# Optimization experiments

Hardware: AMD Instinct MI355X
Metric: run time of the kernel (lower is better)

The kernel has to match this reference:

```python
import jax, jax.numpy as jnp
import numpy as np

N_NODES = 20000

def gcn(h, W, b, src, dst):
    # DGL GraphConv, norm='both': D_out^-1/2 on src, aggregate, D_in^-1/2 on dst, then W, b
    E = src.shape[0]
    ones = jnp.ones((E,), dtype=h.dtype)
    out_deg = jnp.clip(jax.ops.segment_sum(ones, src, N_NODES), 1.0)
    in_deg = jnp.clip(jax.ops.segment_sum(ones, dst, N_NODES), 1.0)
    dn_src = jax.lax.rsqrt(out_deg)  # [N]
    dn_dst = jax.lax.rsqrt(in_deg)
    hs = h * dn_src[None, :, None]           # [B,N,H]
    msg = hs[:, src, :]                      # [B,E,H] gather
    agg = jax.vmap(lambda m: jax.ops.segment_sum(m, dst, N_NODES))(msg)  # [B,N,H]
    agg = agg * dn_dst[None, :, None]
    return agg @ W + b

def setup_inputs() -> dict:
    key = jax.random.key(0)
    ks = jax.random.split(key, 16)
    B, N, H, I, E = 4, N_NODES, 128, 64, 320000
    inp = {
        'x': jax.random.normal(ks[0], (B, I), jnp.float32),
        'h_prev': jax.random.normal(ks[1], (B, N, H), jnp.float32),
        'c_prev': jax.random.normal(ks[2], (B, N, H), jnp.float32),
        'src': jax.random.randint(ks[3], (E,), 0, N, jnp.int32),
        'dst': jax.random.randint(ks[4], (E,), 0, N, jnp.int32),
    }
    s_in = 1.0 / np.sqrt(I)
    s_h = 1.0 / np.sqrt(H)
    inp['Wi'] = jax.random.uniform(ks[5], (I, H), jnp.float32, -s_in, s_in)
    inp['bi'] = jax.random.uniform(ks[6], (H,), jnp.float32, -s_in, s_in)
    inp['Wf'] = jax.random.uniform(ks[7], (I, H), jnp.float32, -s_in, s_in)
    inp['bf'] = jax.random.uniform(ks[8], (H,), jnp.float32, -s_in, s_in)
    inp['Wo'] = jax.random.uniform(ks[9], (I, H), jnp.float32, -s_in, s_in)
    inp['bo'] = jax.random.uniform(ks[10], (H,), jnp.float32, -s_in, s_in)
    inp['Wc'] = jax.random.uniform(ks[11], (I, H), jnp.float32, -s_in, s_in)
    inp['bc'] = jax.random.uniform(ks[12], (H,), jnp.float32, -s_in, s_in)
    inp['Wg'] = jax.random.uniform(ks[13], (H, H), jnp.float32, -s_h, s_h)
    inp['bg'] = jax.random.uniform(ks[14], (H,), jnp.float32, -s_h, s_h)
    return inp

def reference(x, h_prev, c_prev, src, dst, Wi, bi, Wf, bf, Wo, bo, Wc, bc, Wg, bg):
    # gcn_h(g, h_prev) is identical in all four gates -> compute once
    gh = gcn(h_prev, Wg, bg, src, dst)  # [B,N,H]
    i_t = jax.nn.sigmoid((x @ Wi + bi)[:, None, :] + gh)
    f_t = jax.nn.sigmoid((x @ Wf + bf)[:, None, :] + gh)
    o_t = jax.nn.sigmoid((x @ Wo + bo)[:, None, :] + gh)
    c_tilde = jnp.tanh((x @ Wc + bc)[:, None, :] + gh)
    c_t = f_t * c_prev + i_t * c_tilde
    h_t = o_t * jnp.tanh(c_t)
    return h_t, c_t
```

## Files before the change

kernel.cpp:

```cpp
#include <hip/hip_runtime.h>
#include <hip/hip_bf16.h>

#define N_NODES 20000
#define B 4
#define H 128
#define I_DIM 64
#define E_MAX 320000
#define CAP 64

typedef __attribute__((ext_vector_type(8))) short short8;
typedef __attribute__((ext_vector_type(4))) float float4v;

__device__ int   g_cnt_dst[N_NODES];
__device__ int   g_deg_src[N_NODES];
__device__ int   g_csr[N_NODES * CAP];
__device__ float g_xg[4 * B * H];
__device__ __align__(16) uint2 g_hs[N_NODES * H];
__device__ __align__(16) unsigned short g_wgB[H * H];

__global__ __launch_bounds__(256)
void degree_kernel(const int* __restrict__ src, int E, int eb,
                   const float* __restrict__ x,
                   const float* __restrict__ Wi, const float* __restrict__ bi,
                   const float* __restrict__ Wf, const float* __restrict__ bf_,
                   const float* __restrict__ Wo, const float* __restrict__ bo,
                   const float* __restrict__ Wc, const float* __restrict__ bc,
                   const float* __restrict__ Wg) {
    int blk = blockIdx.x;
    int t = threadIdx.x;
    if (blk < eb) {
        int e = blk * 256 + t;
        if (e < E) atomicAdd(&g_deg_src[src[e]], 1);
    } else if (blk < eb + 8) {
        int bid = blk - eb;
        int g = bid >> 1;
        int b = ((bid & 1) << 1) | (t >> 7);
        int h = t & 127;
        const float* W;
        const float* bb;
        switch (g) {
            case 0: W = Wi; bb = bi; break;
            case 1: W = Wf; bb = bf_; break;
            case 2: W = Wo; bb = bo; break;
            default: W = Wc; bb = bc; break;
        }
        float acc = bb[h];
#pragma unroll
        for (int i = 0; i < I_DIM; i++)
            acc += x[b * I_DIM + i] * W[i * H + h];
        g_xg[(g * B + b) * H + h] = acc;
    } else {
        int i = (blk - eb - 8) * 256 + t;
        int tn = i >> 11;
        int rem = i & 2047;
        int kb = rem >> 9;
        int rem2 = rem & 511;
        int lane = rem2 >> 3;
        int j = rem2 & 7;
        int k  = kb * 32 + (lane >> 4) * 8 + j;
        int nn = tn * 16 + (lane & 15);
        __hip_bfloat16 hv = __float2bfloat16(Wg[k * H + nn]);
        g_wgB[i] = *reinterpret_cast<unsigned short*>(&hv);
    }
}

__global__ __launch_bounds__(256)
void mid_kernel(const float* __restrict__ h_prev,
                const int* __restrict__ src, const int* __restrict__ dst, int E) {
    const int PACK_BLKS = (N_NODES * H) / 256;
    int blk = blockIdx.x;
    int t = threadIdx.x;

    if (blk < PACK_BLKS) {
        int i = blk * 256 + t;
        int n = i >> 7;
        float sc = rsqrtf(fmaxf((float)g_deg_src[n], 1.0f));
        const long stride = (long)N_NODES * H;
        float v0 = h_prev[i] * sc;
        float v1 = h_prev[i + stride] * sc;
        float v2 = h_prev[i + 2 * stride] * sc;
        float v3 = h_prev[i + 3 * stride] * sc;
        __hip_bfloat162 p01 = __float22bfloat162_rn(make_float2(v0, v1));
        __hip_bfloat162 p23 = __float22bfloat162_rn(make_float2(v2, v3));
        uint2 wv;
        wv.x = *reinterpret_cast<unsigned int*>(&p01);
        wv.y = *reinterpret_cast<unsigned int*>(&p23);
        g_hs[i] = wv;
    } else {
        int e = (blk - PACK_BLKS) * 256 + t;
        if (e < E) {
            int d = dst[e];
            int slot = atomicAdd(&g_cnt_dst[d], 1);
            if (slot < CAP) g_csr[(d << 6) + slot] = src[e];
        }
    }
}

__device__ __forceinline__ float fast_sigmoid(float z) {
    return 1.f / (1.f + __expf(-z));
}
__device__ __forceinline__ float fast_tanh(float z) {
    return 1.f - 2.f / (__expf(2.f * z) + 1.f);
}
__device__ __forceinline__ unsigned pack2bf(float lo, float hi) {
    __hip_bfloat162 p = __float22bfloat162_rn(make_float2(lo, hi));
    return *reinterpret_cast<unsigned*>(&p);
}

__global__ __launch_bounds__(256)
void fused_kernel(const float* __restrict__ bg,
                  const float* __restrict__ c_prev,
                  float* __restrict__ out_h, float* __restrict__ out_c) {
    int t = threadIdx.x;
    int w = t >> 6;
    int lane = t & 63;
    int n = (blockIdx.x << 2) + w;
    const long stride = (long)N_NODES * H;

    int cnt = g_cnt_dst[n];
    float dd = rsqrtf(fmaxf((float)cnt, 1.0f));
    if (cnt > CAP) cnt = CAP;

    __shared__ int sbase[4][64];
    __shared__ unsigned short Atile[16][136];

    sbase[w][lane] = g_csr[(n << 6) + (lane < cnt ? lane : 0)] << 6;

    float cpr[2][4];
    {
        long ne = (long)((blockIdx.x << 2) + (lane >> 4));
#pragma unroll
        for (int i = 0; i < 2; i++) {
            int h = (2 * w + i) * 16 + (lane & 15);
#pragma unroll
            for (int j = 0; j < 4; j++)
                cpr[i][j] = __builtin_nontemporal_load(
                    &c_prev[(long)j * stride + ne * H + h]);
        }
    }

    float a0 = 0.f, a1 = 0.f, a2 = 0.f, a3 = 0.f;
    float a4 = 0.f, a5 = 0.f, a6 = 0.f, a7 = 0.f;
    const uint4* hs4 = reinterpret_cast<const uint4*>(g_hs);
    const int* sb = sbase[w];

#define ACCV(v) { \
        __hip_bfloat162 p; float2 f; \
        p = *reinterpret_cast<__hip_bfloat162*>(&(v).x); f = __bfloat1622float2(p); a0 += f.x; a1 += f.y; \
        p = *reinterpret_cast<__hip_bfloat162*>(&(v).y); f = __bfloat1622float2(p); a2 += f.x; a3 += f.y; \
        p = *reinterpret_cast<__hip_bfloat162*>(&(v).z); f = __bfloat1622float2(p); a4 += f.x; a5 += f.y; \
        p = *reinterpret_cast<__hip_bfloat162*>(&(v).w); f = __bfloat1622float2(p); a6 += f.x; a7 += f.y; }

    int j = 0;
    for (; j + 8 <= cnt; j += 8) {
        int b0 = sb[j];
        int b1 = sb[j + 1];
        int b2 = sb[j + 2];
        int b3 = sb[j + 3];
        int b4 = sb[j + 4];
        int b5 = sb[j + 5];
        int b6 = sb[j + 6];
        int b7 = sb[j + 7];
        uint4 v0 = hs4[b0 + lane];
        uint4 v1 = hs4[b1 + lane];
        uint4 v2 = hs4[b2 + lane];
        uint4 v3 = hs4[b3 + lane];
        uint4 v4 = hs4[b4 + lane];
        uint4 v5 = hs4[b5 + lane];
        uint4 v6 = hs4[b6 + lane];
        uint4 v7 = hs4[b7 + lane];
        ACCV(v0); ACCV(v1); ACCV(v2); ACCV(v3);
        ACCV(v4); ACCV(v5); ACCV(v6); ACCV(v7);
    }
    for (; j < cnt; j++) {
        uint4 v = hs4[sb[j] + lane];
        ACCV(v);
    }
#undef ACCV

    *reinterpret_cast<unsigned*>(&Atile[w * 4 + 0][2 * lane]) = pack2bf(a0 * dd, a4 * dd);
    *reinterpret_cast<unsigned*>(&Atile[w * 4 + 1][2 * lane]) = pack2bf(a1 * dd, a5 * dd);
    *reinterpret_cast<unsigned*>(&Atile[w * 4 + 2][2 * lane]) = pack2bf(a2 * dd, a6 * dd);
    *reinterpret_cast<unsigned*>(&Atile[w * 4 + 3][2 * lane]) = pack2bf(a3 * dd, a7 * dd);

    __syncthreads();

    if (t < 4)                 g_cnt_dst[(blockIdx.x << 2) + t] = 0;
    else if (t >= 64 && t < 68) g_deg_src[(blockIdx.x << 2) + (t - 64)] = 0;

    int arow = lane & 15;
    int agrp = lane >> 4;
    float4v c0 = {0.f, 0.f, 0.f, 0.f};
    float4v c1 = {0.f, 0.f, 0.f, 0.f};
#pragma unroll
    for (int kb = 0; kb < 4; kb++) {
        short8 af = *reinterpret_cast<const short8*>(&Atile[arow][kb * 32 + agrp * 8]);
        short8 bf0 = *reinterpret_cast<const short8*>(
            &g_wgB[(((2 * w) * 4 + kb) * 64 + lane) * 8]);
        short8 bf1 = *reinterpret_cast<const short8*>(
            &g_wgB[(((2 * w + 1) * 4 + kb) * 64 + lane) * 8]);
        c0 = __builtin_amdgcn_mfma_f32_16x16x32_bf16(af, bf0, c0, 0, 0, 0);
        c1 = __builtin_amdgcn_mfma_f32_16x16x32_bf16(af, bf1, c1, 0, 0, 0);
    }

    long ne = (long)((blockIdx.x << 2) + (lane >> 4));
#pragma unroll
    for (int i = 0; i < 2; i++) {
        float4v c = i ? c1 : c0;
        int h = (2 * w + i) * 16 + (lane & 15);
        float bgh = bg[h];
#pragma unroll
        for (int jj = 0; jj < 4; jj++) {
            float gh = c[jj] + bgh;
            float xi = g_xg[(0 * B + jj) * H + h];
            float xf = g_xg[(1 * B + jj) * H + h];
            float xo = g_xg[(2 * B + jj) * H + h];
            float xc = g_xg[(3 * B + jj) * H + h];

            float it = fast_sigmoid(xi + gh);
            float ft = fast_sigmoid(xf + gh);
            float ot = fast_sigmoid(xo + gh);
            float ct = fast_tanh(xc + gh);

            float cc = ft * cpr[i][jj] + it * ct;
            float ho = ot * fast_tanh(cc);

            long idx = (long)jj * stride + ne * H + h;
            __builtin_nontemporal_store(ho, &out_h[idx]);
            __builtin_nontemporal_store(cc, &out_c[idx]);
        }
    }
}

extern "C" void kernel_launch(void* const* d_in, const int* in_sizes, int n_in,
                              void* d_out, int out_size, void* d_ws, size_t ws_size,
                              hipStream_t stream) {
    const float* x      = (const float*)d_in[0];
    const float* h_prev = (const float*)d_in[1];
    const float* c_prev = (const float*)d_in[2];
    const int* src = (const int*)d_in[3];
    const int* dst = (const int*)d_in[4];
    const float* Wi = (const float*)d_in[5];
    const float* bi = (const float*)d_in[6];
    const float* Wf = (const float*)d_in[7];
    const float* bf_ = (const float*)d_in[8];
    const float* Wo = (const float*)d_in[9];
    const float* bo = (const float*)d_in[10];
    const float* Wc = (const float*)d_in[11];
    const float* bc = (const float*)d_in[12];
    const float* Wg = (const float*)d_in[13];
    const float* bg = (const float*)d_in[14];

    int E = in_sizes[3];
    if (E > E_MAX) E = E_MAX;
    int eb = (E + 255) / 256;
    const int PACK_BLKS = (N_NODES * H) / 256;

    degree_kernel<<<eb + 8 + 64, 256, 0, stream>>>(src, E, eb,
        x, Wi, bi, Wf, bf_, Wo, bo, Wc, bc, Wg);
    mid_kernel<<<PACK_BLKS + eb, 256, 0, stream>>>(h_prev, src, dst, E);

    float* out_h = (float*)d_out;
    float* out_c = out_h + (long)B * N_NODES * H;
    fused_kernel<<<N_NODES / 4, 256, 0, stream>>>(bg, c_prev, out_h, out_c);
}
```

Baseline: 263.2 us.

## Give each wavefront four nodes with full-width MFMA and no block barrier

Each wavefront now gathers neighbour features for four destination nodes and runs the whole 16x128 MFMA tile on its own, so the block-wide __syncthreads is gone and the grid shrinks by four. The gather loop is unrolled to 16 loads, c_prev loads are placed between gather phases to overlap, and the gate inputs are stored interleaved so one float4 load replaces four scalar loads. The cost is higher register pressure (eight accumulator tiles plus 32 cached c_prev values), which may lower occupancy, and fewer blocks overall.

```diff
diff --git a/kernel.cpp b/kernel.cpp
--- a/kernel.cpp
+++ b/kernel.cpp
@@ -14,7 +14,7 @@
 __device__ int   g_cnt_dst[N_NODES];
 __device__ int   g_deg_src[N_NODES];
 __device__ int   g_csr[N_NODES * CAP];
-__device__ float g_xg[4 * B * H];
+__device__ __align__(16) float g_xg[4 * B * H];
 __device__ __align__(16) uint2 g_hs[N_NODES * H];
 __device__ __align__(16) unsigned short g_wgB[H * H];
 
@@ -48,7 +48,7 @@
 #pragma unroll
         for (int i = 0; i < I_DIM; i++)
             acc += x[b * I_DIM + i] * W[i * H + h];
-        g_xg[(g * B + b) * H + h] = acc;
+        g_xg[(b * H + h) * 4 + g] = acc;
     } else {
         int i = (blk - eb - 8) * 256 + t;
         int tn = i >> 11;
@@ -114,33 +114,32 @@
     int t = threadIdx.x;
     int w = t >> 6;
     int lane = t & 63;
-    int n = (blockIdx.x << 2) + w;
+    int q = (blockIdx.x * 4 + w) * 4;
     const long stride = (long)N_NODES * H;
 
-    int cnt = g_cnt_dst[n];
-    float dd = rsqrtf(fmaxf((float)cnt, 1.0f));
-    if (cnt > CAP) cnt = CAP;
-
-    __shared__ int sbase[4][64];
-    __shared__ unsigned short Atile[16][136];
-
-    sbase[w][lane] = g_csr[(n << 6) + (lane < cnt ? lane : 0)] << 6;
-
-    float cpr[2][4];
+    __shared__ int            sbase[4][4 * 64];
+    __shared__ unsigned short Atile[4][16][136];
+
+    int cnt0 = g_cnt_dst[q + 0];
+    int cnt1 = g_cnt_dst[q + 1];
+    int cnt2 = g_cnt_dst[q + 2];
+    int cnt3 = g_cnt_dst[q + 3];
+    float dd0 = rsqrtf(fmaxf((float)cnt0, 1.0f)); if (cnt0 > CAP) cnt0 = CAP;
+    float dd1 = rsqrtf(fmaxf((float)cnt1, 1.0f)); if (cnt1 > CAP) cnt1 = CAP;
+    float dd2 = rsqrtf(fmaxf((float)cnt2, 1.0f)); if (cnt2 > CAP) cnt2 = CAP;
+    float dd3 = rsqrtf(fmaxf((float)cnt3, 1.0f)); if (cnt3 > CAP) cnt3 = CAP;
+
     {
-        long ne = (long)((blockIdx.x << 2) + (lane >> 4));
-#pragma unroll
-        for (int i = 0; i < 2; i++) {
-            int h = (2 * w + i) * 16 + (lane & 15);
-#pragma unroll
-            for (int j = 0; j < 4; j++)
-                cpr[i][j] = __builtin_nontemporal_load(
-                    &c_prev[(long)j * stride + ne * H + h]);
-        }
-    }
-
-    float a0 = 0.f, a1 = 0.f, a2 = 0.f, a3 = 0.f;
-    float a4 = 0.f, a5 = 0.f, a6 = 0.f, a7 = 0.f;
+        int s0 = g_csr[((q + 0) << 6) + (lane < cnt0 ? lane : 0)];
+        int s1 = g_csr[((q + 1) << 6) + (lane < cnt1 ? lane : 0)];
+        int s2 = g_csr[((q + 2) << 6) + (lane < cnt2 ? lane : 0)];
+        int s3 = g_csr[((q + 3) << 6) + (lane < cnt3 ? lane : 0)];
+        sbase[w][0 * 64 + lane] = s0 << 6;
+        sbase[w][1 * 64 + lane] = s1 << 6;
+        sbase[w][2 * 64 + lane] = s2 << 6;
+        sbase[w][3 * 64 + lane] = s3 << 6;
+    }
+
     const uint4* hs4 = reinterpret_cast<const uint4*>(g_hs);
     const int* sb = sbase[w];
 
@@ -151,84 +150,112 @@
         p = *reinterpret_cast<__hip_bfloat162*>(&(v).z); f = __bfloat1622float2(p); a4 += f.x; a5 += f.y; \
         p = *reinterpret_cast<__hip_bfloat162*>(&(v).w); f = __bfloat1622float2(p); a6 += f.x; a7 += f.y; }
 
-    int j = 0;
-    for (; j + 8 <= cnt; j += 8) {
-        int b0 = sb[j];
-        int b1 = sb[j + 1];
-        int b2 = sb[j + 2];
-        int b3 = sb[j + 3];
-        int b4 = sb[j + 4];
-        int b5 = sb[j + 5];
-        int b6 = sb[j + 6];
-        int b7 = sb[j + 7];
-        uint4 v0 = hs4[b0 + lane];
-        uint4 v1 = hs4[b1 + lane];
-        uint4 v2 = hs4[b2 + lane];
-        uint4 v3 = hs4[b3 + lane];
-        uint4 v4 = hs4[b4 + lane];
-        uint4 v5 = hs4[b5 + lane];
-        uint4 v6 = hs4[b6 + lane];
-        uint4 v7 = hs4[b7 + lane];
-        ACCV(v0); ACCV(v1); ACCV(v2); ACCV(v3);
-        ACCV(v4); ACCV(v5); ACCV(v6); ACCV(v7);
-    }
-    for (; j < cnt; j++) {
-        uint4 v = hs4[sb[j] + lane];
-        ACCV(v);
-    }
+#define GATHER_NODE(i, cnt, dd) { \
+        float a0 = 0.f, a1 = 0.f, a2 = 0.f, a3 = 0.f; \
+        float a4 = 0.f, a5 = 0.f, a6 = 0.f, a7 = 0.f; \
+        int j = 0; \
+        for (; j + 16 <= (cnt); j += 16) { \
+            int b0 = sb[(i) * 64 + j];      int b1 = sb[(i) * 64 + j + 1]; \
+            int b2 = sb[(i) * 64 + j + 2];  int b3 = sb[(i) * 64 + j + 3]; \
+            int b4 = sb[(i) * 64 + j + 4];  int b5 = sb[(i) * 64 + j + 5]; \
+            int b6 = sb[(i) * 64 + j + 6];  int b7 = sb[(i) * 64 + j + 7]; \
+            int b8 = sb[(i) * 64 + j + 8];  int b9 = sb[(i) * 64 + j + 9]; \
+            int b10 = sb[(i) * 64 + j + 10]; int b11 = sb[(i) * 64 + j + 11]; \
+            int b12 = sb[(i) * 64 + j + 12]; int b13 = sb[(i) * 64 + j + 13]; \
+            int b14 = sb[(i) * 64 + j + 14]; int b15 = sb[(i) * 64 + j + 15]; \
+            uint4 v0 = hs4[b0 + lane];   uint4 v1 = hs4[b1 + lane]; \
+            uint4 v2 = hs4[b2 + lane];   uint4 v3 = hs4[b3 + lane]; \
+            uint4 v4 = hs4[b4 + lane];   uint4 v5 = hs4[b5 + lane]; \
+            uint4 v6 = hs4[b6 + lane];   uint4 v7 = hs4[b7 + lane]; \
+            uint4 v8 = hs4[b8 + lane];   uint4 v9 = hs4[b9 + lane]; \
+            uint4 v10 = hs4[b10 + lane]; uint4 v11 = hs4[b11 + lane]; \
+            uint4 v12 = hs4[b12 + lane]; uint4 v13 = hs4[b13 + lane]; \
+            uint4 v14 = hs4[b14 + lane]; uint4 v15 = hs4[b15 + lane]; \
+            ACCV(v0);  ACCV(v1);  ACCV(v2);  ACCV(v3); \
+            ACCV(v4);  ACCV(v5);  ACCV(v6);  ACCV(v7); \
+            ACCV(v8);  ACCV(v9);  ACCV(v10); ACCV(v11); \
+            ACCV(v12); ACCV(v13); ACCV(v14); ACCV(v15); \
+        } \
+        for (; j + 4 <= (cnt); j += 4) { \
+            int b0 = sb[(i) * 64 + j];     int b1 = sb[(i) * 64 + j + 1]; \
+            int b2 = sb[(i) * 64 + j + 2]; int b3 = sb[(i) * 64 + j + 3]; \
+            uint4 v0 = hs4[b0 + lane]; uint4 v1 = hs4[b1 + lane]; \
+            uint4 v2 = hs4[b2 + lane]; uint4 v3 = hs4[b3 + lane]; \
+            ACCV(v0); ACCV(v1); ACCV(v2); ACCV(v3); \
+        } \
+        for (; j < (cnt); j++) { \
+            uint4 v = hs4[sb[(i) * 64 + j] + lane]; \
+            ACCV(v); \
+        } \
+        *reinterpret_cast<unsigned*>(&Atile[w][(i) * 4 + 0][2 * lane]) = pack2bf(a0 * (dd), a4 * (dd)); \
+        *reinterpret_cast<unsigned*>(&Atile[w][(i) * 4 + 1][2 * lane]) = pack2bf(a1 * (dd), a5 * (dd)); \
+        *reinterpret_cast<unsigned*>(&Atile[w][(i) * 4 + 2][2 * lane]) = pack2bf(a2 * (dd), a6 * (dd)); \
+        *reinterpret_cast<unsigned*>(&Atile[w][(i) * 4 + 3][2 * lane]) = pack2bf(a3 * (dd), a7 * (dd)); \
+    }
+
+    GATHER_NODE(0, cnt0, dd0);
+    GATHER_NODE(1, cnt1, dd1);
+
+    int hl = lane & 15;
+    long ne = (long)(q + (lane >> 4));
+    float cpr[8][4];
+#pragma unroll
+    for (int tn = 0; tn < 8; tn++) {
+        int h = tn * 16 + hl;
+#pragma unroll
+        for (int jj = 0; jj < 4; jj++)
+            cpr[tn][jj] = __builtin_nontemporal_load(
+                &c_prev[(long)jj * stride + ne * H + h]);
+    }
+
+    GATHER_NODE(2, cnt2, dd2);
+    GATHER_NODE(3, cnt3, dd3);
+#undef GATHER_NODE
 #undef ACCV
-
-    *reinterpret_cast<unsigned*>(&Atile[w * 4 + 0][2 * lane]) = pack2bf(a0 * dd, a4 * dd);
-    *reinterpret_cast<unsigned*>(&Atile[w * 4 + 1][2 * lane]) = pack2bf(a1 * dd, a5 * dd);
-    *reinterpret_cast<unsigned*>(&Atile[w * 4 + 2][2 * lane]) = pack2bf(a2 * dd, a6 * dd);
-    *reinterpret_cast<unsigned*>(&Atile[w * 4 + 3][2 * lane]) = pack2bf(a3 * dd, a7 * dd);
-
-    __syncthreads();
-
-    if (t < 4)                 g_cnt_dst[(blockIdx.x << 2) + t] = 0;
-    else if (t >= 64 && t < 68) g_deg_src[(blockIdx.x << 2) + (t - 64)] = 0;
 
     int arow = lane & 15;
     int agrp = lane >> 4;
-    float4v c0 = {0.f, 0.f, 0.f, 0.f};
-    float4v c1 = {0.f, 0.f, 0.f, 0.f};
+    float4v c[8];
+#pragma unroll
+    for (int tn = 0; tn < 8; tn++) c[tn] = (float4v){0.f, 0.f, 0.f, 0.f};
 #pragma unroll
     for (int kb = 0; kb < 4; kb++) {
-        short8 af = *reinterpret_cast<const short8*>(&Atile[arow][kb * 32 + agrp * 8]);
-        short8 bf0 = *reinterpret_cast<const short8*>(
-            &g_wgB[(((2 * w) * 4 + kb) * 64 + lane) * 8]);
-        short8 bf1 = *reinterpret_cast<const short8*>(
-            &g_wgB[(((2 * w + 1) * 4 + kb) * 64 + lane) * 8]);
-        c0 = __builtin_amdgcn_mfma_f32_16x16x32_bf16(af, bf0, c0, 0, 0, 0);
-        c1 = __builtin_amdgcn_mfma_f32_16x16x32_bf16(af, bf1, c1, 0, 0, 0);
-    }
-
-    long ne = (long)((blockIdx.x << 2) + (lane >> 4));
-#pragma unroll
-    for (int i = 0; i < 2; i++) {
-        float4v c = i ? c1 : c0;
-        int h = (2 * w + i) * 16 + (lane & 15);
+        short8 af = *reinterpret_cast<const short8*>(&Atile[w][arow][kb * 32 + agrp * 8]);
+#pragma unroll
+        for (int tn = 0; tn < 8; tn++) {
+            short8 bf = *reinterpret_cast<const short8*>(
+                &g_wgB[((tn * 4 + kb) * 64 + lane) * 8]);
+            c[tn] = __builtin_amdgcn_mfma_f32_16x16x32_bf16(af, bf, c[tn], 0, 0, 0);
+        }
+    }
+
+    const float4* xg4 = reinterpret_cast<const float4*>(g_xg);
+#pragma unroll
+    for (int tn = 0; tn < 8; tn++) {
+        int h = tn * 16 + hl;
         float bgh = bg[h];
 #pragma unroll
         for (int jj = 0; jj < 4; jj++) {
-            float gh = c[jj] + bgh;
-            float xi = g_xg[(0 * B + jj) * H + h];
-            float xf = g_xg[(1 * B + jj) * H + h];
-            float xo = g_xg[(2 * B + jj) * H + h];
-            float xc = g_xg[(3 * B + jj) * H + h];
-
-            float it = fast_sigmoid(xi + gh);
-            float ft = fast_sigmoid(xf + gh);
-            float ot = fast_sigmoid(xo + gh);
-            float ct = fast_tanh(xc + gh);
-
-            float cc = ft * cpr[i][jj] + it * ct;
+            float gh = c[tn][jj] + bgh;
+            float4 xv = xg4[jj * H + h];
+
+            float it = fast_sigmoid(xv.x + gh);
+            float ft = fast_sigmoid(xv.y + gh);
+            float ot = fast_sigmoid(xv.z + gh);
+            float ct = fast_tanh(xv.w + gh);
+
+            float cc = ft * cpr[tn][jj] + it * ct;
             float ho = ot * fast_tanh(cc);
 
             long idx = (long)jj * stride + ne * H + h;
             __builtin_nontemporal_store(ho, &out_h[idx]);
             __builtin_nontemporal_store(cc, &out_c[idx]);
         }
+    }
+
+    if (lane < 4) {
+        g_cnt_dst[q + lane] = 0;
+        g_deg_src[q + lane] = 0;
     }
 }
 
@@ -262,5 +289,5 @@
 
     float* out_h = (float*)d_out;
     float* out_c = out_h + (long)B * N_NODES * H;
-    fused_kernel<<<N_NODES / 4, 256, 0, stream>>>(bg, c_prev, out_h, out_c);
-}
+    fused_kernel<<<N_NODES / 16, 256, 0, stream>>>(bg, c_prev, out_h, out_c);
+}
```

After: 279.6 us. +6.2%, slower.

## Make each wave compute its own node's GEMM to drop block barrier

Applied to the files above, without the earlier changes.

Each wave now keeps a private A tile filled with its own node's four batch rows replicated across sixteen rows. It runs all eight N-tiles of the Wg matmul itself, so the block-wide __syncthreads is gone and the counter resets happen per wave. The gate inputs g_xg are re-laid out so the four gate values for a (batch, h) pair come in one float4 load, and a 4-wide tail loop is added to the gather. The cost is four times the MFMA work and B-fragment loads per wave, most of it spent on redundant rows, plus four times the shared memory.

```diff
diff --git a/kernel.cpp b/kernel.cpp
--- a/kernel.cpp
+++ b/kernel.cpp
@@ -14,7 +14,7 @@
 __device__ int   g_cnt_dst[N_NODES];
 __device__ int   g_deg_src[N_NODES];
 __device__ int   g_csr[N_NODES * CAP];
-__device__ float g_xg[4 * B * H];
+__device__ __align__(16) float g_xg[4 * B * H];
 __device__ __align__(16) uint2 g_hs[N_NODES * H];
 __device__ __align__(16) unsigned short g_wgB[H * H];
 
@@ -48,7 +48,7 @@
 #pragma unroll
         for (int i = 0; i < I_DIM; i++)
             acc += x[b * I_DIM + i] * W[i * H + h];
-        g_xg[(g * B + b) * H + h] = acc;
+        g_xg[(b * H + h) * 4 + g] = acc;
     } else {
         int i = (blk - eb - 8) * 256 + t;
         int tn = i >> 11;
@@ -117,27 +117,22 @@
     int n = (blockIdx.x << 2) + w;
     const long stride = (long)N_NODES * H;
 
+    __shared__ int            sbase[4][64];
+    __shared__ unsigned short Atile[4][16][136];
+
     int cnt = g_cnt_dst[n];
     float dd = rsqrtf(fmaxf((float)cnt, 1.0f));
     if (cnt > CAP) cnt = CAP;
 
-    __shared__ int sbase[4][64];
-    __shared__ unsigned short Atile[16][136];
-
     sbase[w][lane] = g_csr[(n << 6) + (lane < cnt ? lane : 0)] << 6;
 
     float cpr[2][4];
-    {
-        long ne = (long)((blockIdx.x << 2) + (lane >> 4));
-#pragma unroll
-        for (int i = 0; i < 2; i++) {
-            int h = (2 * w + i) * 16 + (lane & 15);
-#pragma unroll
-            for (int j = 0; j < 4; j++)
-                cpr[i][j] = __builtin_nontemporal_load(
-                    &c_prev[(long)j * stride + ne * H + h]);
-        }
-    }
+#pragma unroll
+    for (int half = 0; half < 2; half++)
+#pragma unroll
+        for (int jj = 0; jj < 4; jj++)
+            cpr[half][jj] = __builtin_nontemporal_load(
+                &c_prev[(long)jj * stride + (long)n * H + 64 * half + lane]);
 
     float a0 = 0.f, a1 = 0.f, a2 = 0.f, a3 = 0.f;
     float a4 = 0.f, a5 = 0.f, a6 = 0.f, a7 = 0.f;
@@ -153,24 +148,23 @@
 
     int j = 0;
     for (; j + 8 <= cnt; j += 8) {
-        int b0 = sb[j];
-        int b1 = sb[j + 1];
-        int b2 = sb[j + 2];
-        int b3 = sb[j + 3];
-        int b4 = sb[j + 4];
-        int b5 = sb[j + 5];
-        int b6 = sb[j + 6];
-        int b7 = sb[j + 7];
-        uint4 v0 = hs4[b0 + lane];
-        uint4 v1 = hs4[b1 + lane];
-        uint4 v2 = hs4[b2 + lane];
-        uint4 v3 = hs4[b3 + lane];
-        uint4 v4 = hs4[b4 + lane];
-        uint4 v5 = hs4[b5 + lane];
-        uint4 v6 = hs4[b6 + lane];
-        uint4 v7 = hs4[b7 + lane];
+        int b0 = sb[j];     int b1 = sb[j + 1];
+        int b2 = sb[j + 2]; int b3 = sb[j + 3];
+        int b4 = sb[j + 4]; int b5 = sb[j + 5];
+        int b6 = sb[j + 6]; int b7 = sb[j + 7];
+        uint4 v0 = hs4[b0 + lane]; uint4 v1 = hs4[b1 + lane];
+        uint4 v2 = hs4[b2 + lane]; uint4 v3 = hs4[b3 + lane];
+        uint4 v4 = hs4[b4 + lane]; uint4 v5 = hs4[b5 + lane];
+        uint4 v6 = hs4[b6 + lane]; uint4 v7 = hs4[b7 + lane];
         ACCV(v0); ACCV(v1); ACCV(v2); ACCV(v3);
         ACCV(v4); ACCV(v5); ACCV(v6); ACCV(v7);
+    }
+    for (; j + 4 <= cnt; j += 4) {
+        int b0 = sb[j];     int b1 = sb[j + 1];
+        int b2 = sb[j + 2]; int b3 = sb[j + 3];
+        uint4 v0 = hs4[b0 + lane]; uint4 v1 = hs4[b1 + lane];
+        uint4 v2 = hs4[b2 + lane]; uint4 v3 = hs4[b3 + lane];
+        ACCV(v0); ACCV(v1); ACCV(v2); ACCV(v3);
     }
     for (; j < cnt; j++) {
         uint4 v = hs4[sb[j] + lane];
@@ -178,58 +172,70 @@
     }
 #undef ACCV
 
-    *reinterpret_cast<unsigned*>(&Atile[w * 4 + 0][2 * lane]) = pack2bf(a0 * dd, a4 * dd);
-    *reinterpret_cast<unsigned*>(&Atile[w * 4 + 1][2 * lane]) = pack2bf(a1 * dd, a5 * dd);
-    *reinterpret_cast<unsigned*>(&Atile[w * 4 + 2][2 * lane]) = pack2bf(a2 * dd, a6 * dd);
-    *reinterpret_cast<unsigned*>(&Atile[w * 4 + 3][2 * lane]) = pack2bf(a3 * dd, a7 * dd);
-
-    __syncthreads();
-
-    if (t < 4)                 g_cnt_dst[(blockIdx.x << 2) + t] = 0;
-    else if (t >= 64 && t < 68) g_deg_src[(blockIdx.x << 2) + (t - 64)] = 0;
+    unsigned p0 = pack2bf(a0 * dd, a4 * dd);
+    unsigned p1 = pack2bf(a1 * dd, a5 * dd);
+    unsigned p2 = pack2bf(a2 * dd, a6 * dd);
+    unsigned p3 = pack2bf(a3 * dd, a7 * dd);
+#pragma unroll
+    for (int r = 0; r < 16; r++) {
+        unsigned pv = ((r & 3) == 0) ? p0 : ((r & 3) == 1) ? p1
+                    : ((r & 3) == 2) ? p2 : p3;
+        *reinterpret_cast<unsigned*>(&Atile[w][r][2 * lane]) = pv;
+    }
 
     int arow = lane & 15;
     int agrp = lane >> 4;
-    float4v c0 = {0.f, 0.f, 0.f, 0.f};
-    float4v c1 = {0.f, 0.f, 0.f, 0.f};
-#pragma unroll
-    for (int kb = 0; kb < 4; kb++) {
-        short8 af = *reinterpret_cast<const short8*>(&Atile[arow][kb * 32 + agrp * 8]);
-        short8 bf0 = *reinterpret_cast<const short8*>(
-            &g_wgB[(((2 * w) * 4 + kb) * 64 + lane) * 8]);
-        short8 bf1 = *reinterpret_cast<const short8*>(
-            &g_wgB[(((2 * w + 1) * 4 + kb) * 64 + lane) * 8]);
-        c0 = __builtin_amdgcn_mfma_f32_16x16x32_bf16(af, bf0, c0, 0, 0, 0);
-        c1 = __builtin_amdgcn_mfma_f32_16x16x32_bf16(af, bf1, c1, 0, 0, 0);
-    }
-
-    long ne = (long)((blockIdx.x << 2) + (lane >> 4));
-#pragma unroll
-    for (int i = 0; i < 2; i++) {
-        float4v c = i ? c1 : c0;
-        int h = (2 * w + i) * 16 + (lane & 15);
+    int g = lane >> 4;
+    const float4* xg4 = reinterpret_cast<const float4*>(g_xg);
+
+#pragma unroll
+    for (int half = 0; half < 2; half++) {
+        float4v c0 = {0.f, 0.f, 0.f, 0.f};
+        float4v c1 = {0.f, 0.f, 0.f, 0.f};
+        float4v c2 = {0.f, 0.f, 0.f, 0.f};
+        float4v c3 = {0.f, 0.f, 0.f, 0.f};
+#pragma unroll
+        for (int kb = 0; kb < 4; kb++) {
+            short8 af = *reinterpret_cast<const short8*>(
+                &Atile[w][arow][kb * 32 + agrp * 8]);
+            short8 b0 = *reinterpret_cast<const short8*>(
+                &g_wgB[(((4 * half + 0) * 4 + kb) * 64 + lane) * 8]);
+            short8 b1 = *reinterpret_cast<const short8*>(
+                &g_wgB[(((4 * half + 1) * 4 + kb) * 64 + lane) * 8]);
+            short8 b2 = *reinterpret_cast<const short8*>(
+                &g_wgB[(((4 * half + 2) * 4 + kb) * 64 + lane) * 8]);
+            short8 b3 = *reinterpret_cast<const short8*>(
+                &g_wgB[(((4 * half + 3) * 4 + kb) * 64 + lane) * 8]);
+            c0 = __builtin_amdgcn_mfma_f32_16x16x32_bf16(af, b0, c0, 0, 0, 0);
+            c1 = __builtin_amdgcn_mfma_f32_16x16x32_bf16(af, b1, c1, 0, 0, 0);
+            c2 = __builtin_amdgcn_mfma_f32_16x16x32_bf16(af, b2, c2, 0, 0, 0);
+            c3 = __builtin_amdgcn_mfma_f32_16x16x32_bf16(af, b3, c3, 0, 0, 0);
+        }
+        float4v mine = (g == 0) ? c0 : (g == 1) ? c1 : (g == 2) ? c2 : c3;
+
+        int h = 64 * half + lane;
         float bgh = bg[h];
 #pragma unroll
         for (int jj = 0; jj < 4; jj++) {
-            float gh = c[jj] + bgh;
-            float xi = g_xg[(0 * B + jj) * H + h];
-            float xf = g_xg[(1 * B + jj) * H + h];
-            float xo = g_xg[(2 * B + jj) * H + h];
-            float xc = g_xg[(3 * B + jj) * H + h];
-
-            float it = fast_sigmoid(xi + gh);
-            float ft = fast_sigmoid(xf + gh);
-            float ot = fast_sigmoid(xo + gh);
-            float ct = fast_tanh(xc + gh);
-
-            float cc = ft * cpr[i][jj] + it * ct;
+            float gh = mine[jj] + bgh;
+            float4 xv = xg4[jj * H + h];
+
+            float it = fast_sigmoid(xv.x + gh);
+            float ft = fast_sigmoid(xv.y + gh);
+            float ot = fast_sigmoid(xv.z + gh);
+            float ct = fast_tanh(xv.w + gh);
+
+            float cc = ft * cpr[half][jj] + it * ct;
             float ho = ot * fast_tanh(cc);
 
-            long idx = (long)jj * stride + ne * H + h;
+            long idx = (long)jj * stride + (long)n * H + h;
             __builtin_nontemporal_store(ho, &out_h[idx]);
             __builtin_nontemporal_store(cc, &out_c[idx]);
         }
     }
+
+    if (lane == 0) g_cnt_dst[n] = 0;
+    if (lane == 1) g_deg_src[n] = 0;
 }
 
 extern "C" void kernel_launch(void* const* d_in, const int* in_sizes, int n_in,
```

Result: no change. 261.2 us (-0.8%).
